# Optimization experiments

Hardware: AMD Instinct MI355X
Metric: run time of the kernel (lower is better)

Reference implementation:

```python
import jax, jax.numpy as jnp
import numpy as np

B, SE, HE, DE = 32, 256, 512, 2
HD = DE * HE            # decoder hidden (h0 reshape implies Hd = De*He)
ED = 256                # label embedding dim
N = 8192                # seq label num (output_size)
T = 20                  # decode_max_seq_len (eval path)
KE = VE = 1024
MD = 256
EIN = ED + HE           # LSTM input size
EOS_ID = 0
SPARCE_RATE = 0.8
NEG = -1.0e7
MAXV = 1.0e9
EPS = 1e-8


def setup_inputs() -> dict:
    key = jax.random.key(0)
    ks = jax.random.split(key, 20)
    s = 0.05
    return {
        'encoded_hidden_embeddings': jax.random.normal(ks[0], (B, SE, HE), jnp.float32),
        'hidden': jax.random.normal(ks[1], (DE, B, HE), jnp.float32),
        'cell': jax.random.normal(ks[2], (DE, B, HE), jnp.float32),
        'text_lengths': jax.random.randint(ks[3], (B,), 1, SE + 1),
        'encoder_mask': jnp.ones((B, SE), bool),
        'memory_key_mask': jnp.ones((B, KE), bool),
        'memory_key_embedding': jax.random.normal(ks[4], (B, KE, MD), jnp.float32),
        'memory_value_mask': jnp.ones((B, VE), bool),
        'memory_value_embedding': jax.random.normal(ks[5], (B, VE, MD), jnp.float32),
        # parameters
        'W_ih': jax.random.normal(ks[6], (4 * HD, EIN), jnp.float32) * s,
        'W_hh': jax.random.normal(ks[7], (4 * HD, HD), jnp.float32) * s,
        'b_ih': jnp.zeros((4 * HD,), jnp.float32),
        'b_hh': jnp.zeros((4 * HD,), jnp.float32),
        'mlp_W1': jax.random.normal(ks[8], (HD, HD), jnp.float32) * s,
        'mlp_b1': jnp.zeros((HD,), jnp.float32),
        'mlp_W2': jax.random.normal(ks[9], (N, HD), jnp.float32) * s,
        'mlp_b2': jnp.zeros((N,), jnp.float32),
        'emb_table': jax.random.normal(ks[10], (N, ED), jnp.float32) * s,
        'dense_W': jax.random.normal(ks[11], (HE, ED), jnp.float32) * s,
        'dense_b': jnp.zeros((HE,), jnp.float32),
        'read_W': jax.random.normal(ks[12], (MD, EIN), jnp.float32) * s,
        'read_b': jnp.zeros((MD,), jnp.float32),
    }


def _cos(a, b):
    num = jnp.sum(a * b, axis=-1)
    den = jnp.maximum(jnp.linalg.norm(a, axis=-1) * jnp.linalg.norm(b, axis=-1), EPS)
    return num / den


def _lstm(x, h, c, W_ih, W_hh, b_ih, b_hh):
    g = x @ W_ih.T + b_ih + h @ W_hh.T + b_hh
    i, f, gg, o = jnp.split(g, 4, axis=-1)  # torch gate order i,f,g,o
    c1 = jax.nn.sigmoid(f) * c + jax.nn.sigmoid(i) * jnp.tanh(gg)
    h1 = jax.nn.sigmoid(o) * jnp.tanh(c1)
    return h1, c1


def _forward(enc, hidden, cell, encoder_mask, memory_key_mask, memory_value_mask,
             mem_k, mem_v, W_ih, W_hh, b_ih, b_hh, mlp_W1, mlp_b1, mlp_W2, mlp_b2,
             emb_table, dense_W, dense_b, read_W, read_b):
    h0 = jnp.transpose(hidden, (1, 0, 2)).reshape(B, HD)
    c0 = jnp.transpose(cell, (1, 0, 2)).reshape(B, HD)
    pad = jnp.where(encoder_mask, 0.0, -MAXV).astype(enc.dtype)  # (B,Se)
    sent = enc[:, 0, :]                                           # (B,He)
    x0 = jnp.zeros((B, EIN), enc.dtype)
    mask0 = jnp.zeros((B, N), enc.dtype)

    def step(carry, _):
        h, c, x, lmask = carry
        h, c = _lstm(x, h, c, W_ih, W_hh, b_ih, b_hh)
        hid = jax.nn.relu(h @ mlp_W1.T + mlp_b1)
        logits = hid @ mlp_W2.T + mlp_b2 + lmask          # (B,N)
        nid = jnp.argmax(logits, axis=-1)                 # (B,) greedy decode
        lab = emb_table[nid]                              # (B,Ed)
        lmask = lmask.at[jnp.arange(B), nid].set(NEG)     # scatter-mask used ids
        lmask = lmask.at[:, EOS_ID].set(0.0)              # EOS always allowed
        q = lab @ dense_W.T + dense_b                     # (B,He)
        score = jnp.einsum('bse,be->bs', enc, q) + pad
        w = jax.nn.softmax(score, axis=-1)
        attn = jnp.einsum('bse,bs->be', enc, w)
        x = jnp.concatenate([lab, sent + attn], axis=-1)  # (B,Ed+He)
        mq = x @ read_W.T + read_b                        # (B,Md)
        ksim = _cos(mq[:, None, :], mem_k)                # (B,Ke)
        return (h, c, x, lmask), (logits, nid, ksim)

    _, (outputs, next_ids, key_sims) = jax.lax.scan(step, (h0, c0, x0, mask0), None, length=T)
    outputs = jnp.transpose(outputs, (1, 0, 2))           # (B,T,N)
    next_ids = next_ids.T                                 # (B,T)
    key_sims = jnp.transpose(key_sims, (1, 0, 2))         # (B,T,Ke)

    key_sim = jnp.max(key_sims, axis=1)                   # (B,Ke)
    key_sim = jnp.where(key_sim < 0, 0.0, key_sim)
    # mapping_weight: pairwise cosine between memory keys and values (B,Ke,Ve)
    mw = _cos(mem_k[:, :, None, :], mem_v[:, None, :, :])
    keep = (mw >= jnp.max(mw, axis=-1, keepdims=True)) & (mw >= SPARCE_RATE)
    mw = jnp.where(keep, mw, 0.0)
    val_sim = jnp.einsum('bk,bkv->bv', key_sim, mw)       # (B,Ve)
    key_out = jnp.where(memory_key_mask, key_sim, -1.0)
    val_out = jnp.where(memory_value_mask, val_sim, -1.0)
    return outputs, next_ids, key_out, val_out


def reference(encoded_hidden_embeddings, hidden, cell, text_lengths, encoder_mask,
              memory_key_mask, memory_key_embedding, memory_value_mask, memory_value_embedding,
              W_ih, W_hh, b_ih, b_hh, mlp_W1, mlp_b1, mlp_W2, mlp_b2,
              emb_table, dense_W, dense_b, read_W, read_b):
    del text_lengths  # unused in module math
    return _forward(encoded_hidden_embeddings, hidden, cell, encoder_mask,
                    memory_key_mask, memory_value_mask, memory_key_embedding,
                    memory_value_embedding, W_ih, W_hh, b_ih, b_hh,
                    mlp_W1, mlp_b1, mlp_W2, mlp_b2, emb_table,
                    dense_W, dense_b, read_W, read_b)
```

## Files before the change

kernel.cpp:

```cpp
#include <hip/hip_runtime.h>
#include <cstdint>
#include <cstddef>

#define B_   32
#define SE_  256
#define HE_  512
#define HD_  1024
#define ED_  256
#define N_   8192
#define T_   20
#define KE_  1024
#define VE_  1024
#define MD_  256
#define EIN_ 768
#define NEG_   (-10000000.0f)
#define MAXV_  (1000000000.0f)
#define EPS_   (1e-8f)
#define SPARSE_ 0.8f
#define GATE_  0.78f

#define NLOGB (N_/16)

#define O_IDS  (B_*T_*N_)
#define O_KEY  (O_IDS + B_*T_)
#define O_VAL  (O_KEY + B_*KE_)

typedef __attribute__((ext_vector_type(8))) short short8;
typedef __attribute__((ext_vector_type(4))) float floatx4;

__device__ __forceinline__ float sigf(float v) { return 1.0f / (1.0f + expf(-v)); }

__device__ __forceinline__ short f2bf(float f) {
    union { float f; unsigned u; } v; v.f = f;
    unsigned r = v.u + 0x7FFFu + ((v.u >> 16) & 1u);
    return (short)(r >> 16);
}
__device__ __forceinline__ short8 pack8(const float4 a, const float4 b) {
    short8 r;
    r[0]=f2bf(a.x); r[1]=f2bf(a.y); r[2]=f2bf(a.z); r[3]=f2bf(a.w);
    r[4]=f2bf(b.x); r[5]=f2bf(b.y); r[6]=f2bf(b.z); r[7]=f2bf(b.w);
    return r;
}

__device__ __forceinline__ bool mask_is_b8(const void* p) {
    unsigned u = *(const unsigned*)p;
    return u > 0xFFu;
}
__device__ __forceinline__ bool mask_at(const void* p, int idx, bool b8) {
    return b8 ? (((const unsigned char*)p)[idx] != 0)
              : (((const int*)p)[idx] != 0);
}

__global__ __launch_bounds__(256) void k_init(
    const float* __restrict__ hidden, const float* __restrict__ cell,
    const float* __restrict__ enc, const void* __restrict__ encmask,
    float* __restrict__ h, float* __restrict__ c, float* __restrict__ x,
    float* __restrict__ lmask, float* __restrict__ sent, float* __restrict__ pad,
    float* __restrict__ key_run, float* __restrict__ val_sim, float* __restrict__ rowmax)
{
    int idx = blockIdx.x * 256 + threadIdx.x;
    lmask[idx] = 0.0f;
    if (idx < B_ * HD_) {
        int b = idx >> 10, j = idx & 1023;
        int d = j >> 9, e = j & 511;
        h[idx] = hidden[((size_t)d * B_ + b) * HE_ + e];
        c[idx] = cell  [((size_t)d * B_ + b) * HE_ + e];
        key_run[idx] = -1e30f;
        val_sim[idx] = 0.0f;
        rowmax[idx] = 0.0f;
    }
    if (idx < B_ * EIN_) x[idx] = 0.0f;
    if (idx < B_ * HE_) {
        int b = idx >> 9, e = idx & 511;
        sent[idx] = enc[(size_t)b * SE_ * HE_ + e];
    }
    if (idx < B_ * SE_) {
        bool b8 = mask_is_b8(encmask);
        pad[idx] = mask_at(encmask, idx, b8) ? 0.0f : -MAXV_;
    }
}

__global__ __launch_bounds__(256) void k_norms(
    const float* __restrict__ mem_k, const float* __restrict__ mem_v,
    float* __restrict__ normk, float* __restrict__ normv)
{
    int lane = threadIdx.x & 63;
    int wave = (blockIdx.x * 256 + threadIdx.x) >> 6;
    for (int row = wave; row < 2 * B_ * KE_; row += 1024) {
        const float* base = (row < B_ * KE_) ? (mem_k + (size_t)row * MD_)
                                             : (mem_v + (size_t)(row - B_ * KE_) * MD_);
        float4 v = ((const float4*)base)[lane];
        float s = v.x*v.x + v.y*v.y + v.z*v.z + v.w*v.w;
        for (int m = 32; m; m >>= 1) s += __shfl_xor(s, m, 64);
        if (lane == 0) {
            if (row < B_ * KE_) normk[row] = sqrtf(s);
            else                normv[row - B_ * KE_] = sqrtf(s);
        }
    }
}

__global__ __launch_bounds__(256) void k_rowmax_mfma(
    const float* __restrict__ mem_k, const float* __restrict__ mem_v,
    const float* __restrict__ normk, const float* __restrict__ normv,
    float* __restrict__ rowmax)
{
    __shared__ __align__(16) short Vs[64 * 256];
    const int tid = threadIdx.x, lane = tid & 63, w = tid >> 6;
    const int kt = blockIdx.x, vseg = blockIdx.y, b = blockIdx.z;
    const int rowbase = kt * 128 + w * 32;
    const int lrow = lane & 15, lq = lane >> 4;

    float nk[2][4];
    #pragma unroll
    for (int rg = 0; rg < 2; ++rg)
        #pragma unroll
        for (int reg = 0; reg < 4; ++reg)
            nk[rg][reg] = normk[b * KE_ + rowbase + rg * 16 + lq * 4 + reg];

    short8 af[2][8];
    #pragma unroll
    for (int rg = 0; rg < 2; ++rg) {
        const float* arow = mem_k + ((size_t)(b * KE_ + rowbase + rg * 16 + lrow)) * MD_;
        #pragma unroll
        for (int kc = 0; kc < 8; ++kc) {
            const float* p = arow + kc * 32 + lq * 8;
            float4 f0 = *(const float4*)p;
            float4 f1 = *(const float4*)(p + 4);
            af[rg][kc] = pack8(f0, f1);
        }
    }

    float rmax[2][4];
    #pragma unroll
    for (int rg = 0; rg < 2; ++rg)
        #pragma unroll
        for (int reg = 0; reg < 4; ++reg) rmax[rg][reg] = -1e30f;

    for (int vs = vseg * 4; vs < vseg * 4 + 4; ++vs) {
        __syncthreads();
        #pragma unroll
        for (int i = 0; i < 8; ++i) {
            int lin = tid + i * 256;
            int r = lin >> 5, cg = lin & 31;
            const float* p = mem_v + ((size_t)(b * VE_ + vs * 64 + r)) * MD_ + cg * 8;
            float4 f0 = *(const float4*)p;
            float4 f1 = *(const float4*)(p + 4);
            int byt = (r * 512 + cg * 16) ^ ((r & 7) << 4);
            *(short8*)((char*)Vs + byt) = pack8(f0, f1);
        }
        __syncthreads();

        for (int vsub = 0; vsub < 4; ++vsub) {
            int vrow = vsub * 16 + lrow;
            float nv = normv[b * VE_ + vs * 64 + vrow];
            short8 bfr[8];
            #pragma unroll
            for (int kc = 0; kc < 8; ++kc) {
                int byt = (vrow * 512 + kc * 64 + lq * 16) ^ ((vrow & 7) << 4);
                bfr[kc] = *(const short8*)((char*)Vs + byt);
            }
            #pragma unroll
            for (int rg = 0; rg < 2; ++rg) {
                floatx4 acc = {0.0f, 0.0f, 0.0f, 0.0f};
                #pragma unroll
                for (int kc = 0; kc < 8; ++kc)
                    acc = __builtin_amdgcn_mfma_f32_16x16x32_bf16(af[rg][kc], bfr[kc], acc, 0, 0, 0);
                #pragma unroll
                for (int reg = 0; reg < 4; ++reg) {
                    float cs = acc[reg] / fmaxf(nk[rg][reg] * nv, EPS_);
                    rmax[rg][reg] = fmaxf(rmax[rg][reg], cs);
                }
            }
        }
    }
    #pragma unroll
    for (int rg = 0; rg < 2; ++rg)
        #pragma unroll
        for (int reg = 0; reg < 4; ++reg) {
            float v = rmax[rg][reg];
            v = fmaxf(v, __shfl_xor(v, 1, 64));
            v = fmaxf(v, __shfl_xor(v, 2, 64));
            v = fmaxf(v, __shfl_xor(v, 4, 64));
            v = fmaxf(v, __shfl_xor(v, 8, 64));
            if (lrow == 0) {
                int* p = (int*)&rowmax[(size_t)b * KE_ + rowbase + rg * 16 + lq * 4 + reg];
                atomicMax(p, __float_as_int(fmaxf(v, 0.0f)));
            }
        }
}

__device__ __forceinline__ float wave_dot(const float* __restrict__ row, const float* vl, int quads)
{
    int lane = threadIdx.x & 63;
    float s = 0.0f;
    for (int q = lane; q < quads; q += 64) {
        float4 a = ((const float4*)row)[q];
        float4 x = ((const float4*)vl)[q];
        s = fmaf(a.x, x.x, s); s = fmaf(a.y, x.y, s);
        s = fmaf(a.z, x.z, s); s = fmaf(a.w, x.w, s);
    }
    for (int m = 32; m; m >>= 1) s += __shfl_xor(s, m, 64);
    return s;
}

__global__ __launch_bounds__(256) void k_gates_ksim(
    const float* __restrict__ x, const float* __restrict__ W_ih,
    const float* __restrict__ h_in, const float* __restrict__ W_hh,
    const float* __restrict__ b_ih, const float* __restrict__ b_hh,
    float* __restrict__ c_st, float* __restrict__ h_out,
    const float* __restrict__ mqg, const float* __restrict__ mem_k,
    const float* __restrict__ normk, float* __restrict__ key_run, int do_ksim)
{
    __shared__ __align__(16) float Xs[32 * 256];
    __shared__ float red[8][32][17];
    const int tid = threadIdx.x;

    if (blockIdx.x >= 512) {
        if (!do_ksim) return;
        float* mql  = Xs;
        float* red2 = Xs + 256;
        const int u = blockIdx.x - 512;
        const int kt = u & 15, b = u >> 4;
        const int lane = tid & 63, w = tid >> 6;
        float mv = mqg[(size_t)b * MD_ + tid];
        mql[tid] = mv;
        red2[tid] = mv * mv;
        __syncthreads();
        for (int s = 128; s > 0; s >>= 1) { if (tid < s) red2[tid] += red2[tid + s]; __syncthreads(); }
        float nmq = sqrtf(red2[0]);
        int base = kt * 64 + w * 16;
        for (int i = 0; i < 16; ++i) {
            int k = base + i;
            float num = wave_dot(mem_k + ((size_t)b * KE_ + k) * MD_, mql, MD_ / 4);
            if (lane == 0) {
                float cs = num / fmaxf(nmq * normk[b * KE_ + k], EPS_);
                float o = key_run[b * KE_ + k];
                key_run[b * KE_ + k] = fmaxf(o, cs);
            }
        }
        return;
    }

    const int kg = tid & 15, jg = (tid >> 4) & 3, bg = tid >> 6;
    const int ch0 = blockIdx.x * 2;

    float acc[2][8];
    #pragma unroll
    for (int jv = 0; jv < 2; ++jv)
        #pragma unroll
        for (int bv = 0; bv < 8; ++bv) acc[jv][bv] = 0.0f;

    for (int k0 = 0; k0 < EIN_ + HD_; k0 += 256) {
        const bool second = (k0 >= EIN_);
        const float* Xsrc = second ? h_in : x;
        const float* Wsrc = second ? W_hh : W_ih;
        const int srcK = second ? HD_ : EIN_;
        const int ks = second ? (k0 - EIN_) : k0;
        __syncthreads();
        #pragma unroll
        for (int i = 0; i < 8; ++i) {
            int lin = tid + i * 256;
            int bb = lin >> 6, q = lin & 63;
            *(float4*)&Xs[bb * 256 + q * 4] = *(const float4*)(Xsrc + (size_t)bb * srcK + ks + q * 4);
        }
        __syncthreads();
        #pragma unroll
        for (int qq = 0; qq < 4; ++qq) {
            const int qc = kg + qq * 16;
            float4 wv[2];
            #pragma unroll
            for (int jv = 0; jv < 2; ++jv) {
                int row = jg * HD_ + ch0 + jv;
                wv[jv] = *(const float4*)(Wsrc + (size_t)row * srcK + ks + qc * 4);
            }
            #pragma unroll
            for (int bv = 0; bv < 8; ++bv) {
                float4 x4 = *(const float4*)&Xs[(bg * 8 + bv) * 256 + qc * 4];
                #pragma unroll
                for (int jv = 0; jv < 2; ++jv) {
                    acc[jv][bv] = fmaf(wv[jv].x, x4.x, acc[jv][bv]);
                    acc[jv][bv] = fmaf(wv[jv].y, x4.y, acc[jv][bv]);
                    acc[jv][bv] = fmaf(wv[jv].z, x4.z, acc[jv][bv]);
                    acc[jv][bv] = fmaf(wv[jv].w, x4.w, acc[jv][bv]);
                }
            }
        }
    }
    #pragma unroll
    for (int jv = 0; jv < 2; ++jv)
        #pragma unroll
        for (int bv = 0; bv < 8; ++bv)
            red[jg * 2 + jv][bg * 8 + bv][kg] = acc[jv][bv];
    __syncthreads();
    if (tid < 64) {
        const int c2 = tid >> 5, b = tid & 31;
        float g4[4];
        #pragma unroll
        for (int gate = 0; gate < 4; ++gate) {
            float s = 0.0f;
            #pragma unroll
            for (int k = 0; k < 16; ++k) s += red[gate * 2 + c2][b][k];
            int row = gate * HD_ + ch0 + c2;
            g4[gate] = s + b_ih[row] + b_hh[row];
        }
        int idx = b * HD_ + ch0 + c2;
        float c1 = sigf(g4[1]) * c_st[idx] + sigf(g4[0]) * tanhf(g4[2]);
        h_out[idx] = sigf(g4[3]) * tanhf(c1);
        c_st[idx] = c1;
    }
}

__global__ __launch_bounds__(256) void k_mlp1(
    const float* __restrict__ X, const float* __restrict__ W,
    const float* __restrict__ bias, float* __restrict__ out)
{
    __shared__ __align__(16) float Xs[32 * 256];
    __shared__ float red[4][32][17];
    const int tid = threadIdx.x;
    const int kg = tid & 15, jg = (tid >> 4) & 3, bg = tid >> 6;
    const int jbase = blockIdx.x * 4;

    float acc[8];
    #pragma unroll
    for (int bv = 0; bv < 8; ++bv) acc[bv] = 0.0f;

    for (int k0 = 0; k0 < HD_; k0 += 256) {
        __syncthreads();
        #pragma unroll
        for (int i = 0; i < 8; ++i) {
            int lin = tid + i * 256;
            int bb = lin >> 6, q = lin & 63;
            *(float4*)&Xs[bb * 256 + q * 4] = *(const float4*)(X + (size_t)bb * HD_ + k0 + q * 4);
        }
        __syncthreads();
        #pragma unroll
        for (int qq = 0; qq < 4; ++qq) {
            const int qc = kg + qq * 16;
            float4 w4 = *(const float4*)(W + (size_t)(jbase + jg) * HD_ + k0 + qc * 4);
            #pragma unroll
            for (int bv = 0; bv < 8; ++bv) {
                float4 x4 = *(const float4*)&Xs[(bg * 8 + bv) * 256 + qc * 4];
                acc[bv] = fmaf(w4.x, x4.x, acc[bv]);
                acc[bv] = fmaf(w4.y, x4.y, acc[bv]);
                acc[bv] = fmaf(w4.z, x4.z, acc[bv]);
                acc[bv] = fmaf(w4.w, x4.w, acc[bv]);
            }
        }
    }
    #pragma unroll
    for (int bv = 0; bv < 8; ++bv)
        red[jg][bg * 8 + bv][kg] = acc[bv];
    __syncthreads();
    if (tid < 128) {
        int jjo = tid >> 5, b = tid & 31;
        float s = 0.0f;
        #pragma unroll
        for (int k = 0; k < 16; ++k) s += red[jjo][b][k];
        int jo = jbase + jjo;
        out[(size_t)b * HD_ + jo] = fmaxf(s + bias[jo], 0.0f);
    }
}

__global__ __launch_bounds__(256) void k_logits(
    const float* __restrict__ hid, const float* __restrict__ W2,
    const float* __restrict__ b2, const float* __restrict__ lmask,
    float* __restrict__ lg_out, float* __restrict__ pval, int* __restrict__ pidx)
{
    __shared__ __align__(16) float Xs[32 * 256];
    __shared__ float red[16][32][17];
    const int tid = threadIdx.x;
    const int kg = tid & 15, jg = (tid >> 4) & 3, bg = tid >> 6;
    const int jbase = blockIdx.x * 16;

    float acc[4][8];
    #pragma unroll
    for (int jv = 0; jv < 4; ++jv)
        #pragma unroll
        for (int bv = 0; bv < 8; ++bv) acc[jv][bv] = 0.0f;

    for (int k0 = 0; k0 < HD_; k0 += 256) {
        __syncthreads();
        #pragma unroll
        for (int i = 0; i < 8; ++i) {
            int lin = tid + i * 256;
            int bb = lin >> 6, q = lin & 63;
            *(float4*)&Xs[bb * 256 + q * 4] = *(const float4*)(hid + (size_t)bb * HD_ + k0 + q * 4);
        }
        __syncthreads();
        #pragma unroll
        for (int qq = 0; qq < 4; ++qq) {
            const int qc = kg + qq * 16;
            float4 wv[4];
            #pragma unroll
            for (int jv = 0; jv < 4; ++jv)
                wv[jv] = *(const float4*)(W2 + (size_t)(jbase + jg * 4 + jv) * HD_ + k0 + qc * 4);
            #pragma unroll
            for (int bv = 0; bv < 8; ++bv) {
                float4 x4 = *(const float4*)&Xs[(bg * 8 + bv) * 256 + qc * 4];
                #pragma unroll
                for (int jv = 0; jv < 4; ++jv) {
                    acc[jv][bv] = fmaf(wv[jv].x, x4.x, acc[jv][bv]);
                    acc[jv][bv] = fmaf(wv[jv].y, x4.y, acc[jv][bv]);
                    acc[jv][bv] = fmaf(wv[jv].z, x4.z, acc[jv][bv]);
                    acc[jv][bv] = fmaf(wv[jv].w, x4.w, acc[jv][bv]);
                }
            }
        }
    }
    #pragma unroll
    for (int jv = 0; jv < 4; ++jv)
        #pragma unroll
        for (int bv = 0; bv < 8; ++bv)
            red[jg * 4 + jv][bg * 8 + bv][kg] = acc[jv][bv];
    __syncthreads();
    for (int o = tid; o < 16 * B_; o += 256) {
        int jjo = o >> 5, b = o & 31;
        float s = 0.0f;
        #pragma unroll
        for (int k = 0; k < 16; ++k) s += red[jjo][b][k];
        int jo = jbase + jjo;
        s += b2[jo] + lmask[(size_t)b * N_ + jo];
        lg_out[(size_t)b * (T_ * N_) + jo] = s;
        red[jjo][b][16] = s;
    }
    __syncthreads();
    if (tid < 32) {
        int b = tid;
        float best = -1e38f; int bi = 0;
        #pragma unroll
        for (int jjo = 0; jjo < 16; ++jjo) {
            float v = red[jjo][b][16];
            if (v > best) { best = v; bi = jjo; }
        }
        pval[(size_t)b * NLOGB + blockIdx.x] = best;
        pidx[(size_t)b * NLOGB + blockIdx.x] = jbase + bi;
    }
}

__global__ __launch_bounds__(256) void k_merge(
    const float* __restrict__ pval, const int* __restrict__ pidx,
    float* __restrict__ d_out, int t, int* __restrict__ nidbuf,
    float* __restrict__ lmask, const float* __restrict__ emb,
    const float* __restrict__ dense_W, const float* __restrict__ dense_b,
    float* __restrict__ qbuf)
{
    __shared__ float sv[256];
    __shared__ int   si[256];
    __shared__ __align__(16) float lab[ED_];
    const int b = blockIdx.x, tid = threadIdx.x;
    float best = -1e38f; int bi = N_;
    for (int p = tid; p < NLOGB; p += 256) {
        float v = pval[(size_t)b * NLOGB + p];
        int   i = pidx[(size_t)b * NLOGB + p];
        if (v > best || (v == best && i < bi)) { best = v; bi = i; }
    }
    sv[tid] = best; si[tid] = bi;
    __syncthreads();
    for (int s = 128; s > 0; s >>= 1) {
        if (tid < s) {
            float v2 = sv[tid + s]; int i2 = si[tid + s];
            if (v2 > sv[tid] || (v2 == sv[tid] && i2 < si[tid])) { sv[tid] = v2; si[tid] = i2; }
        }
        __syncthreads();
    }
    int nid = si[0];
    if (tid == 0) {
        nidbuf[b] = nid;
        d_out[O_IDS + (size_t)b * T_ + t] = (float)nid;
        lmask[(size_t)b * N_ + nid] = NEG_;
        lmask[(size_t)b * N_] = 0.0f;
    }
    lab[tid] = emb[(size_t)nid * ED_ + tid];
    __syncthreads();
    const float4* Lq = (const float4*)lab;
    #pragma unroll
    for (int jj = 0; jj < 2; ++jj) {
        int j = tid + jj * 256;
        const float4* Wq = (const float4*)(dense_W + (size_t)j * ED_);
        float s0 = 0.0f, s1 = 0.0f, s2 = 0.0f, s3 = 0.0f;
        #pragma unroll
        for (int q = 0; q < 64; q += 4) {
            float4 w0 = Wq[q],   x0 = Lq[q];
            float4 w1 = Wq[q+1], x1 = Lq[q+1];
            float4 w2 = Wq[q+2], x2 = Lq[q+2];
            float4 w3 = Wq[q+3], x3 = Lq[q+3];
            s0 = fmaf(w0.x,x0.x,s0); s0 = fmaf(w0.y,x0.y,s0); s0 = fmaf(w0.z,x0.z,s0); s0 = fmaf(w0.w,x0.w,s0);
            s1 = fmaf(w1.x,x1.x,s1); s1 = fmaf(w1.y,x1.y,s1); s1 = fmaf(w1.z,x1.z,s1); s1 = fmaf(w1.w,x1.w,s1);
            s2 = fmaf(w2.x,x2.x,s2); s2 = fmaf(w2.y,x2.y,s2); s2 = fmaf(w2.z,x2.z,s2); s2 = fmaf(w2.w,x2.w,s2);
            s3 = fmaf(w3.x,x3.x,s3); s3 = fmaf(w3.y,x3.y,s3); s3 = fmaf(w3.z,x3.z,s3); s3 = fmaf(w3.w,x3.w,s3);
        }
        qbuf[(size_t)b * HE_ + j] = dense_b[j] + ((s0 + s1) + (s2 + s3));
    }
}

__global__ __launch_bounds__(256) void k_attn1(
    const float* __restrict__ qg, const float* __restrict__ enc,
    const float* __restrict__ pad, float* __restrict__ part)
{
    __shared__ __align__(16) float ql[HE_];
    __shared__ float sc_l[32];
    __shared__ float wp_l[32];
    const int b = blockIdx.y, sc = blockIdx.x;
    const int tid = threadIdx.x, lane = tid & 63, w = tid >> 6;
    ql[tid] = qg[(size_t)b * HE_ + tid];
    ql[tid + 256] = qg[(size_t)b * HE_ + tid + 256];
    __syncthreads();

    #pragma unroll
    for (int i = 0; i < 8; ++i) {
        int sl = w + i * 4;
        int s = sc * 32 + sl;
        float v = wave_dot(enc + ((size_t)b * SE_ + s) * HE_, ql, HE_ / 4);
        if (lane == 0) sc_l[sl] = v + pad[b * SE_ + s];
    }
    __syncthreads();

    float m = -1e38f;
    #pragma unroll
    for (int i = 0; i < 32; ++i) m = fmaxf(m, sc_l[i]);
    if (tid < 32) wp_l[tid] = expf(sc_l[tid] - m);
    __syncthreads();
    float esum = 0.0f;
    #pragma unroll
    for (int i = 0; i < 32; ++i) esum += wp_l[i];

    float a0 = 0.0f, a1 = 0.0f;
    for (int i = 0; i < 32; ++i) {
        float wv = wp_l[i];
        const float* er = enc + ((size_t)b * SE_ + sc * 32 + i) * HE_;
        a0 = fmaf(wv, er[tid], a0);
        a1 = fmaf(wv, er[tid + 256], a1);
    }
    float* pb = part + ((size_t)b * 8 + sc) * 516;
    pb[tid] = a0;
    pb[256 + tid] = a1;
    if (tid == 0) { pb[512] = m; pb[513] = esum; }
}

__global__ __launch_bounds__(256) void k_attn2read(
    const float* __restrict__ part, const float* __restrict__ sent,
    const int* __restrict__ nidbuf, const float* __restrict__ emb,
    const float* __restrict__ read_W, const float* __restrict__ read_b,
    float* __restrict__ xg, float* __restrict__ mqg)
{
    __shared__ float ms[8], es[8];
    __shared__ __align__(16) float xl[EIN_];
    const int qv = blockIdx.x, b = blockIdx.y;
    const int tid = threadIdx.x;
    if (tid < 8) {
        ms[tid] = part[((size_t)b * 8 + tid) * 516 + 512];
        es[tid] = part[((size_t)b * 8 + tid) * 516 + 513];
    }
    __syncthreads();
    float m = -1e38f;
    #pragma unroll
    for (int c = 0; c < 8; ++c) m = fmaxf(m, ms[c]);
    float scale[8];
    float denom = 0.0f;
    #pragma unroll
    for (int c = 0; c < 8; ++c) { scale[c] = expf(ms[c] - m); denom += es[c] * scale[c]; }
    float inv = 1.0f / denom;
    float a0 = 0.0f, a1 = 0.0f;
    #pragma unroll
    for (int c = 0; c < 8; ++c) {
        const float* pb = part + ((size_t)b * 8 + c) * 516;
        a0 = fmaf(scale[c], pb[tid], a0);
        a1 = fmaf(scale[c], pb[256 + tid], a1);
    }
    a0 *= inv; a1 *= inv;
    int nid = nidbuf[b];
    xl[tid]             = emb[(size_t)nid * ED_ + tid];
    xl[ED_ + tid]       = sent[(size_t)b * HE_ + tid]       + a0;
    xl[ED_ + 256 + tid] = sent[(size_t)b * HE_ + 256 + tid] + a1;
    __syncthreads();
    if (qv == 0) {
        float* xr = xg + (size_t)b * EIN_;
        xr[tid] = xl[tid]; xr[tid + 256] = xl[tid + 256]; xr[tid + 512] = xl[tid + 512];
    }
    const int r = qv * 64 + (tid >> 2), kq = tid & 3;
    const float4* Wq = (const float4*)(read_W + (size_t)r * EIN_ + kq * 192);
    const float4* xq = (const float4*)(xl + kq * 192);
    float s0 = 0.0f, s1 = 0.0f, s2 = 0.0f, s3 = 0.0f;
    #pragma unroll
    for (int q = 0; q < 48; q += 4) {
        float4 w0 = Wq[q],   v0 = xq[q];
        float4 w1 = Wq[q+1], v1 = xq[q+1];
        float4 w2 = Wq[q+2], v2 = xq[q+2];
        float4 w3 = Wq[q+3], v3 = xq[q+3];
        s0 = fmaf(w0.x,v0.x,s0); s0 = fmaf(w0.y,v0.y,s0); s0 = fmaf(w0.z,v0.z,s0); s0 = fmaf(w0.w,v0.w,s0);
        s1 = fmaf(w1.x,v1.x,s1); s1 = fmaf(w1.y,v1.y,s1); s1 = fmaf(w1.z,v1.z,s1); s1 = fmaf(w1.w,v1.w,s1);
        s2 = fmaf(w2.x,v2.x,s2); s2 = fmaf(w2.y,v2.y,s2); s2 = fmaf(w2.z,v2.z,s2); s2 = fmaf(w2.w,v2.w,s2);
        s3 = fmaf(w3.x,v3.x,s3); s3 = fmaf(w3.z,v3.z,s3); s3 = fmaf(w3.y,v3.y,s3); s3 = fmaf(w3.w,v3.w,s3);
    }
    float s = ((s0 + s1) + (s2 + s3));
    s += __shfl_xor(s, 1, 64);
    s += __shfl_xor(s, 2, 64);
    if (kq == 0) mqg[(size_t)b * MD_ + r] = s + read_b[r];
}

__global__ __launch_bounds__(256) void k_ksim(
    const float* __restrict__ mqg,
    const float* __restrict__ mem_k, const float* __restrict__ normk,
    float* __restrict__ key_run)
{
    __shared__ __align__(16) float mql[MD_];
    __shared__ float red[256];
    const int b = blockIdx.y, kt = blockIdx.x;
    const int tid = threadIdx.x, lane = tid & 63, w = tid >> 6;
    float mv = mqg[(size_t)b * MD_ + tid];
    mql[tid] = mv;
    red[tid] = mv * mv;
    __syncthreads();
    for (int s = 128; s > 0; s >>= 1) { if (tid < s) red[tid] += red[tid + s]; __syncthreads(); }
    float nmq = sqrtf(red[0]);

    int base = kt * 64 + w * 16;
    for (int i = 0; i < 16; ++i) {
        int k = base + i;
        float num = wave_dot(mem_k + ((size_t)b * KE_ + k) * MD_, mql, MD_ / 4);
        if (lane == 0) {
            float cs = num / fmaxf(nmq * normk[b * KE_ + k], EPS_);
            float o = key_run[b * KE_ + k];
            key_run[b * KE_ + k] = fmaxf(o, cs);
        }
    }
}

__global__ __launch_bounds__(256) void k_keyfinal(
    float* __restrict__ key_run, const void* __restrict__ kmask, float* __restrict__ d_out)
{
    int idx = blockIdx.x * 256 + threadIdx.x;
    bool b8 = mask_is_b8(kmask);
    float v = key_run[idx];
    v = (v < 0.0f) ? 0.0f : v;
    key_run[idx] = v;
    d_out[O_KEY + idx] = mask_at(kmask, idx, b8) ? v : -1.0f;
}

__global__ __launch_bounds__(256) void k_val(
    const float* __restrict__ rowmax, const float* __restrict__ mem_k, const float* __restrict__ mem_v,
    const float* __restrict__ normk, const float* __restrict__ normv,
    const float* __restrict__ key_sim, float* __restrict__ val_sim)
{
    int idx = blockIdx.x * 256 + threadIdx.x;
    if (rowmax[idx] < GATE_) return;
    int b = idx >> 10;
    const float* krow = mem_k + (size_t)idx * MD_;
    float nk = normk[idx];
    float ks = key_sim[idx];
    float rm = -1e30f;
    for (int v = 0; v < VE_; ++v) {
        const float* vrow = mem_v + ((size_t)b * VE_ + v) * MD_;
        float d = 0.0f;
        for (int e = 0; e < MD_; ++e) d = fmaf(krow[e], vrow[e], d);
        float cs = d / fmaxf(nk * normv[b * VE_ + v], EPS_);
        rm = fmaxf(rm, cs);
    }
    float thr = fmaxf(rm, SPARSE_);
    for (int v = 0; v < VE_; ++v) {
        const float* vrow = mem_v + ((size_t)b * VE_ + v) * MD_;
        float d = 0.0f;
        for (int e = 0; e < MD_; ++e) d = fmaf(krow[e], vrow[e], d);
        float cs = d / fmaxf(nk * normv[b * VE_ + v], EPS_);
        if (cs >= thr) atomicAdd(&val_sim[(size_t)b * VE_ + v], ks * cs);
    }
}

__global__ __launch_bounds__(256) void k_valout(
    const float* __restrict__ val_sim, const void* __restrict__ vmask, float* __restrict__ d_out)
{
    int idx = blockIdx.x * 256 + threadIdx.x;
    bool b8 = mask_is_b8(vmask);
    d_out[O_VAL + idx] = mask_at(vmask, idx, b8) ? val_sim[idx] : -1.0f;
}

extern "C" void kernel_launch(void* const* d_in, const int* in_sizes, int n_in,
                              void* d_out_v, int out_size, void* d_ws, size_t ws_size,
                              hipStream_t stream)
{
    const float* enc      = (const float*)d_in[0];
    const float* hidden   = (const float*)d_in[1];
    const float* cell     = (const float*)d_in[2];
    const void*  encmask  = d_in[4];
    const void*  kmask    = d_in[5];
    const float* mem_k    = (const float*)d_in[6];
    const void*  vmask    = d_in[7];
    const float* mem_v    = (const float*)d_in[8];
    const float* W_ih     = (const float*)d_in[9];
    const float* W_hh     = (const float*)d_in[10];
    const float* b_ih     = (const float*)d_in[11];
    const float* b_hh     = (const float*)d_in[12];
    const float* mlp_W1   = (const float*)d_in[13];
    const float* mlp_b1   = (const float*)d_in[14];
    const float* mlp_W2   = (const float*)d_in[15];
    const float* mlp_b2   = (const float*)d_in[16];
    const float* emb      = (const float*)d_in[17];
    const float* dense_W  = (const float*)d_in[18];
    const float* dense_b  = (const float*)d_in[19];
    const float* read_W   = (const float*)d_in[20];
    const float* read_b   = (const float*)d_in[21];
    float* d_out = (float*)d_out_v;
    float* ws = (float*)d_ws;

    float* hA      = ws;
    float* hB      = ws + 32768;
    float* c       = ws + 65536;
    float* x       = ws + 98304;
    float* hid     = ws + 122880;
    float* lmask   = ws + 155648;
    float* sent    = ws + 417792;
    float* pad     = ws + 434176;
    float* key_run = ws + 442368;
    float* val_sim = ws + 475136;
    float* normk   = ws + 507904;
    float* normv   = ws + 540672;
    float* rowmax  = ws + 573440;
    int*   nidbuf  = (int*)(ws + 606208);
    float* mqg     = ws + 606272;
    float* qbuf    = ws + 614464;
    float* part    = ws + 630848;
    float* pval    = ws + 762944;
    int*   pidx    = (int*)(ws + 779328);

    k_init<<<1024, 256, 0, stream>>>(hidden, cell, enc, encmask, hA, c, x, lmask, sent, pad, key_run, val_sim, rowmax);
    k_norms<<<256, 256, 0, stream>>>(mem_k, mem_v, normk, normv);
    k_rowmax_mfma<<<dim3(8, 4, 32), 256, 0, stream>>>(mem_k, mem_v, normk, normv, rowmax);

    const float* hin = hA;
    float* hout = hB;
    for (int t = 0; t < T_; ++t) {
        k_gates_ksim<<<1024, 256, 0, stream>>>(x, W_ih, hin, W_hh, b_ih, b_hh, c, hout,
                                               mqg, mem_k, normk, key_run, t > 0 ? 1 : 0);
        k_mlp1<<<HD_ / 4, 256, 0, stream>>>(hout, mlp_W1, mlp_b1, hid);
        k_logits<<<N_ / 16, 256, 0, stream>>>(hid, mlp_W2, mlp_b2, lmask,
                                              d_out + (size_t)t * N_, pval, pidx);
        k_merge<<<B_, 256, 0, stream>>>(pval, pidx, d_out, t, nidbuf, lmask,
                                        emb, dense_W, dense_b, qbuf);
        k_attn1<<<dim3(8, B_), 256, 0, stream>>>(qbuf, enc, pad, part);
        k_attn2read<<<dim3(4, B_), 256, 0, stream>>>(part, sent, nidbuf, emb, read_W, read_b, x, mqg);
        float* tmp = (float*)hin; hin = hout; hout = tmp;
    }
    k_ksim<<<dim3(16, B_), 256, 0, stream>>>(mqg, mem_k, normk, key_run);

    k_keyfinal<<<128, 256, 0, stream>>>(key_run, kmask, d_out);
    k_val<<<128, 256, 0, stream>>>(rowmax, mem_k, mem_v, normk, normv, key_run, val_sim);
    k_valout<<<128, 256, 0, stream>>>(val_sim, vmask, d_out);
}
```

Before: 2.552 ms.

## Replace two-pass argmax with packed 64-bit atomicMax and fuse merge into attention

The logits kernel now publishes each block's best value and index as a single order-preserving 64-bit key through atomicMax into a per-step slot. This removes the partial-result buffers and the separate merge kernel. The attention kernel reads the winning id directly, recomputes the dense query projection per block, and performs the lmask/id bookkeeping from one block. That saves one launch and one reduction pass per step, in exchange for redundant dense_W matvec work across the 8 attention blocks per batch row and contended atomics.

Result: slower. 2.793 ms (+9.4%).

```diff
diff --git a/kernel.cpp b/kernel.cpp
--- a/kernel.cpp
+++ b/kernel.cpp
@@ -42,6 +42,11 @@
     return r;
 }
 
+__device__ __forceinline__ unsigned ord_f(float f) {
+    unsigned u = __float_as_uint(f);
+    return (u & 0x80000000u) ? ~u : (u | 0x80000000u);
+}
+
 __device__ __forceinline__ bool mask_is_b8(const void* p) {
     unsigned u = *(const unsigned*)p;
     return u > 0xFFu;
@@ -56,10 +61,12 @@
     const float* __restrict__ enc, const void* __restrict__ encmask,
     float* __restrict__ h, float* __restrict__ c, float* __restrict__ x,
     float* __restrict__ lmask, float* __restrict__ sent, float* __restrict__ pad,
-    float* __restrict__ key_run, float* __restrict__ val_sim, float* __restrict__ rowmax)
+    float* __restrict__ key_run, float* __restrict__ val_sim, float* __restrict__ rowmax,
+    unsigned long long* __restrict__ amax)
 {
     int idx = blockIdx.x * 256 + threadIdx.x;
     lmask[idx] = 0.0f;
+    if (idx < T_ * B_) amax[idx] = 0ULL;
     if (idx < B_ * HD_) {
         int b = idx >> 10, j = idx & 1023;
         int d = j >> 9, e = j & 511;
@@ -364,7 +371,7 @@
 __global__ __launch_bounds__(256) void k_logits(
     const float* __restrict__ hid, const float* __restrict__ W2,
     const float* __restrict__ b2, const float* __restrict__ lmask,
-    float* __restrict__ lg_out, float* __restrict__ pval, int* __restrict__ pidx)
+    float* __restrict__ lg_out, unsigned long long* __restrict__ amax_t)
 {
     __shared__ __align__(16) float Xs[32 * 256];
     __shared__ float red[16][32][17];
@@ -432,39 +439,29 @@
             float v = red[jjo][b][16];
             if (v > best) { best = v; bi = jjo; }
         }
-        pval[(size_t)b * NLOGB + blockIdx.x] = best;
-        pidx[(size_t)b * NLOGB + blockIdx.x] = jbase + bi;
-    }
-}
-
-__global__ __launch_bounds__(256) void k_merge(
-    const float* __restrict__ pval, const int* __restrict__ pidx,
+        unsigned long long packed =
+            ((unsigned long long)ord_f(best) << 32) | (unsigned)(N_ - 1 - (jbase + bi));
+        atomicMax(&amax_t[b], packed);
+    }
+}
+
+__global__ __launch_bounds__(256) void k_attn1m(
+    const unsigned long long* __restrict__ amax_t,
+    const float* __restrict__ emb, const float* __restrict__ dense_W,
+    const float* __restrict__ dense_b,
+    const float* __restrict__ enc, const float* __restrict__ pad,
     float* __restrict__ d_out, int t, int* __restrict__ nidbuf,
-    float* __restrict__ lmask, const float* __restrict__ emb,
-    const float* __restrict__ dense_W, const float* __restrict__ dense_b,
-    float* __restrict__ qbuf)
-{
-    __shared__ float sv[256];
-    __shared__ int   si[256];
+    float* __restrict__ lmask, float* __restrict__ part)
+{
     __shared__ __align__(16) float lab[ED_];
-    const int b = blockIdx.x, tid = threadIdx.x;
-    float best = -1e38f; int bi = N_;
-    for (int p = tid; p < NLOGB; p += 256) {
-        float v = pval[(size_t)b * NLOGB + p];
-        int   i = pidx[(size_t)b * NLOGB + p];
-        if (v > best || (v == best && i < bi)) { best = v; bi = i; }
-    }
-    sv[tid] = best; si[tid] = bi;
-    __syncthreads();
-    for (int s = 128; s > 0; s >>= 1) {
-        if (tid < s) {
-            float v2 = sv[tid + s]; int i2 = si[tid + s];
-            if (v2 > sv[tid] || (v2 == sv[tid] && i2 < si[tid])) { sv[tid] = v2; si[tid] = i2; }
-        }
-        __syncthreads();
-    }
-    int nid = si[0];
-    if (tid == 0) {
+    __shared__ __align__(16) float ql[HE_];
+    __shared__ float sc_l[32];
+    __shared__ float wp_l[32];
+    const int b = blockIdx.y, sc = blockIdx.x;
+    const int tid = threadIdx.x, lane = tid & 63, w = tid >> 6;
+
+    const int nid = N_ - 1 - (int)(amax_t[b] & 0xFFFFFFFFULL);
+    if (sc == 0 && tid == 0) {
         nidbuf[b] = nid;
         d_out[O_IDS + (size_t)b * T_ + t] = (float)nid;
         lmask[(size_t)b * N_ + nid] = NEG_;
@@ -472,6 +469,7 @@
     }
     lab[tid] = emb[(size_t)nid * ED_ + tid];
     __syncthreads();
+
     const float4* Lq = (const float4*)lab;
     #pragma unroll
     for (int jj = 0; jj < 2; ++jj) {
@@ -489,21 +487,8 @@
             s2 = fmaf(w2.x,x2.x,s2); s2 = fmaf(w2.y,x2.y,s2); s2 = fmaf(w2.z,x2.z,s2); s2 = fmaf(w2.w,x2.w,s2);
             s3 = fmaf(w3.x,x3.x,s3); s3 = fmaf(w3.y,x3.y,s3); s3 = fmaf(w3.z,x3.z,s3); s3 = fmaf(w3.w,x3.w,s3);
         }
-        qbuf[(size_t)b * HE_ + j] = dense_b[j] + ((s0 + s1) + (s2 + s3));
-    }
-}
-
-__global__ __launch_bounds__(256) void k_attn1(
-    const float* __restrict__ qg, const float* __restrict__ enc,
-    const float* __restrict__ pad, float* __restrict__ part)
-{
-    __shared__ __align__(16) float ql[HE_];
-    __shared__ float sc_l[32];
-    __shared__ float wp_l[32];
-    const int b = blockIdx.y, sc = blockIdx.x;
-    const int tid = threadIdx.x, lane = tid & 63, w = tid >> 6;
-    ql[tid] = qg[(size_t)b * HE_ + tid];
-    ql[tid + 256] = qg[(size_t)b * HE_ + tid + 256];
+        ql[j] = dense_b[j] + ((s0 + s1) + (s2 + s3));
+    }
     __syncthreads();
 
     #pragma unroll
@@ -717,12 +702,11 @@
     float* rowmax  = ws + 573440;
     int*   nidbuf  = (int*)(ws + 606208);
     float* mqg     = ws + 606272;
-    float* qbuf    = ws + 614464;
     float* part    = ws + 630848;
-    float* pval    = ws + 762944;
-    int*   pidx    = (int*)(ws + 779328);
-
-    k_init<<<1024, 256, 0, stream>>>(hidden, cell, enc, encmask, hA, c, x, lmask, sent, pad, key_run, val_sim, rowmax);
+    unsigned long long* amax = (unsigned long long*)(ws + 762944);
+
+    k_init<<<1024, 256, 0, stream>>>(hidden, cell, enc, encmask, hA, c, x, lmask, sent, pad,
+                                     key_run, val_sim, rowmax, amax);
     k_norms<<<256, 256, 0, stream>>>(mem_k, mem_v, normk, normv);
     k_rowmax_mfma<<<dim3(8, 4, 32), 256, 0, stream>>>(mem_k, mem_v, normk, normv, rowmax);
 
@@ -733,10 +717,9 @@
                                                mqg, mem_k, normk, key_run, t > 0 ? 1 : 0);
         k_mlp1<<<HD_ / 4, 256, 0, stream>>>(hout, mlp_W1, mlp_b1, hid);
         k_logits<<<N_ / 16, 256, 0, stream>>>(hid, mlp_W2, mlp_b2, lmask,
-                                              d_out + (size_t)t * N_, pval, pidx);
-        k_merge<<<B_, 256, 0, stream>>>(pval, pidx, d_out, t, nidbuf, lmask,
-                                        emb, dense_W, dense_b, qbuf);
-        k_attn1<<<dim3(8, B_), 256, 0, stream>>>(qbuf, enc, pad, part);
+                                              d_out + (size_t)t * N_, amax + (size_t)t * B_);
+        k_attn1m<<<dim3(8, B_), 256, 0, stream>>>(amax + (size_t)t * B_, emb, dense_W, dense_b,
+                                                  enc, pad, d_out, t, nidbuf, lmask, part);
         k_attn2read<<<dim3(4, B_), 256, 0, stream>>>(part, sent, nidbuf, emb, read_W, read_b, x, mqg);
         float* tmp = (float*)hin; hin = hout; hout = tmp;
     }
```
